# Optimization experiments

Measured on AMD Instinct MI355X. Metric: run time of the kernel, lower is better.

Reference implementation:

```python
import jax, jax.numpy as jnp
import numpy as np

MARGIN = 1.0
EPS = 1e-12


def setup_inputs() -> dict:
    key = jax.random.key(0)
    k1, k2 = jax.random.split(key)
    embeddings = jax.random.normal(k1, (4096, 768), dtype=jnp.float32)
    labels = jax.random.randint(k2, (4096,), 0, 4, dtype=jnp.int64)
    return {"embeddings": embeddings, "labels": labels}


def reference(embeddings, labels):
    # F.normalize(p=2, dim=1): x / max(||x||, eps)
    norm = jnp.linalg.norm(embeddings, axis=1, keepdims=True)
    e = embeddings / jnp.maximum(norm, EPS)

    # Euclidean pairwise distance matrix (not squared)
    dot = e @ e.T                                  # [N, N]
    sq = jnp.diagonal(dot)                         # [N]
    dist = sq[None, :] - 2.0 * dot + sq[:, None]
    dist = jnp.sqrt(jnp.maximum(dist, 0.0) + EPS)  # [N, N]

    # Masks: positives = same label, off-diagonal; negatives = different label
    n = labels.shape[0]
    eq = labels[None, :] == labels[:, None]
    pos_mask = eq & ~jnp.eye(n, dtype=bool)
    neg_mask = ~eq

    # Batch-hard mining: per-anchor hardest positive (masked max) and
    # hardest negative (masked min) -- replaces the per-row Python loop.
    d_ap = jnp.max(jnp.where(pos_mask, dist, -jnp.inf), axis=1)  # [N]
    d_an = jnp.min(jnp.where(neg_mask, dist, jnp.inf), axis=1)   # [N]

    valid = jnp.any(pos_mask, axis=1)  # anchors with at least one positive
    per_anchor = jnp.maximum(d_ap - d_an + MARGIN, 0.0)
    per_anchor = jnp.where(valid, per_anchor, 0.0)
    n_valid = jnp.maximum(jnp.sum(valid.astype(jnp.float32)), 1.0)
    return jnp.sum(per_anchor) / n_valid
```

## Files before the change

kernel.cpp:

```cpp
#include <hip/hip_runtime.h>
#include <math.h>

#define N 4096
#define D 768
#define MARGIN 1.0f
#define NBLK 576
#define NKT 24

typedef _Float16 half8 __attribute__((ext_vector_type(8)));
typedef _Float16 half4 __attribute__((ext_vector_type(4)));
typedef float f32x4 __attribute__((ext_vector_type(4)));

__device__ __forceinline__ void gl2lds16(const void* g, void* l) {
    __builtin_amdgcn_global_load_lds((const __attribute__((address_space(1))) void*)g,
                                     (__attribute__((address_space(3))) void*)l, 16, 0, 0);
}

template<int Nv>
__device__ __forceinline__ void wait_vm() {
    if constexpr (Nv == 0)      asm volatile("s_waitcnt vmcnt(0)" ::: "memory");
    else if constexpr (Nv == 3) asm volatile("s_waitcnt vmcnt(3)" ::: "memory");
    else                        asm volatile("s_waitcnt vmcnt(4)" ::: "memory");
}

__global__ __launch_bounds__(256) void normalize_kernel(const float* __restrict__ x,
                                                        _Float16* __restrict__ e,
                                                        float* __restrict__ sq,
                                                        unsigned* __restrict__ ap_bits,
                                                        unsigned* __restrict__ an_bits,
                                                        unsigned* __restrict__ counter) {
    const int tid = threadIdx.x;
    const int wave = tid >> 6, lane = tid & 63;
    const int row = blockIdx.x * 4 + wave;

    const float4* xr = (const float4*)(x + (size_t)row * D);
    float4 f0 = xr[lane];
    float4 f1 = xr[lane + 64];
    float4 f2 = xr[lane + 128];

    float s = f0.x*f0.x + f0.y*f0.y + f0.z*f0.z + f0.w*f0.w
            + f1.x*f1.x + f1.y*f1.y + f1.z*f1.z + f1.w*f1.w
            + f2.x*f2.x + f2.y*f2.y + f2.z*f2.z + f2.w*f2.w;
    #pragma unroll
    for (int off = 1; off < 64; off <<= 1) s += __shfl_xor(s, off, 64);

    float scale = 1.0f / fmaxf(sqrtf(s), 1e-12f);

    half4* er = (half4*)(e + (size_t)row * D);
    half4 h0 = { (_Float16)(f0.x*scale), (_Float16)(f0.y*scale), (_Float16)(f0.z*scale), (_Float16)(f0.w*scale) };
    half4 h1 = { (_Float16)(f1.x*scale), (_Float16)(f1.y*scale), (_Float16)(f1.z*scale), (_Float16)(f1.w*scale) };
    half4 h2 = { (_Float16)(f2.x*scale), (_Float16)(f2.y*scale), (_Float16)(f2.z*scale), (_Float16)(f2.w*scale) };
    er[lane]       = h0;
    er[lane + 64]  = h1;
    er[lane + 128] = h2;

    if (lane == 0) {
        sq[row] = s * scale * scale;
        ap_bits[row] = 0u;
        an_bits[row] = 0x7f800000u;
    }
    if (blockIdx.x == 0 && tid == 0) *counter = 0u;
}

template<int BROWS>
__device__ __forceinline__ void stage_tile(const _Float16* __restrict__ e,
                                           int i0, int jbase, int k0,
                                           unsigned short* Sb, int tid, int w) {
    #pragma unroll
    for (int p = 0; p < 2; ++p) {
        int s  = p * 256 + tid;
        int r  = s >> 2;
        int kg = (s & 3) ^ ((r >> 1) & 3);
        gl2lds16(e + (size_t)(i0 + r) * D + k0 + kg * 8,
                 (char*)Sb + (p * 256 + w * 64) * 16);
    }
    if constexpr (BROWS == 128) {
        #pragma unroll
        for (int p = 0; p < 2; ++p) {
            int s  = p * 256 + tid;
            int r  = s >> 2;
            int kg = (s & 3) ^ ((r >> 1) & 3);
            gl2lds16(e + (size_t)(jbase + r) * D + k0 + kg * 8,
                     (char*)Sb + 8192 + (p * 256 + w * 64) * 16);
        }
    } else {
        int s  = tid & 127;
        int r  = s >> 2;
        int kg = (s & 3) ^ ((r >> 1) & 3);
        gl2lds16(e + (size_t)(jbase + r) * D + k0 + kg * 8,
                 (char*)Sb + 8192 + ((w & 1) * 64) * 16);
    }
}

template<int MTN, int NTN, int BROWS>
__device__ __forceinline__ void tile_work(const _Float16* __restrict__ e,
                                          const float* __restrict__ sq,
                                          const int* __restrict__ labels,
                                          unsigned* __restrict__ ap_bits,
                                          unsigned* __restrict__ an_bits,
                                          unsigned short* S,
                                          int i0, int jbase,
                                          int wi, int wjL,
                                          int tid, int w, int lane, bool diag) {
    const int ln15 = lane & 15;
    const int lq   = lane >> 4;
    constexpr int LPS = (BROWS == 128) ? 4 : 3;

    f32x4 acc[MTN][NTN] = {};

    stage_tile<BROWS>(e, i0, jbase, 0,  S,        tid, w);
    stage_tile<BROWS>(e, i0, jbase, 32, S + 8192, tid, w);

    int cur = 0, nx2 = 2;
    for (int kt = 0; kt < NKT; ++kt) {
        if (kt < NKT - 1) wait_vm<LPS>(); else wait_vm<0>();
        __builtin_amdgcn_s_barrier();
        __builtin_amdgcn_sched_barrier(0);

        if (kt + 2 < NKT)
            stage_tile<BROWS>(e, i0, jbase, (kt + 2) * 32, S + nx2 * 8192, tid, w);
        __builtin_amdgcn_sched_barrier(0);

        const unsigned short* Sb = S + cur * 8192;
        half8 af[MTN], bf[NTN];
        #pragma unroll
        for (int mt = 0; mt < MTN; ++mt) {
            int r  = wi + mt * 16 + ln15;
            int kx = lq ^ ((r >> 1) & 3);
            af[mt] = *(const half8*)&Sb[r * 32 + kx * 8];
        }
        #pragma unroll
        for (int nt = 0; nt < NTN; ++nt) {
            int r  = wjL + nt * 16 + ln15;
            int kx = lq ^ ((r >> 1) & 3);
            bf[nt] = *(const half8*)&Sb[4096 + r * 32 + kx * 8];
        }
        __builtin_amdgcn_s_setprio(1);
        #pragma unroll
        for (int mt = 0; mt < MTN; ++mt)
            #pragma unroll
            for (int nt = 0; nt < NTN; ++nt)
                acc[mt][nt] = __builtin_amdgcn_mfma_f32_16x16x32_f16(af[mt], bf[nt], acc[mt][nt], 0, 0, 0);
        __builtin_amdgcn_s_setprio(0);

        cur = (cur == 2) ? 0 : cur + 1;
        nx2 = (nx2 == 2) ? 0 : nx2 + 1;
    }

    float sqi[MTN][4]; int labi[MTN][4];
    #pragma unroll
    for (int mt = 0; mt < MTN; ++mt)
        #pragma unroll
        for (int rg = 0; rg < 4; ++rg) {
            int i = i0 + wi + mt * 16 + lq * 4 + rg;
            sqi[mt][rg] = sq[i];
            labi[mt][rg] = labels[i];
        }
    float sqj[NTN]; int labj[NTN];
    #pragma unroll
    for (int nt = 0; nt < NTN; ++nt) {
        int j = jbase + wjL + nt * 16 + ln15;
        sqj[nt] = sq[j];
        labj[nt] = labels[j];
    }

    float api[MTN][4], ani[MTN][4], apj[NTN], anj[NTN];
    #pragma unroll
    for (int mt = 0; mt < MTN; ++mt)
        #pragma unroll
        for (int rg = 0; rg < 4; ++rg) { api[mt][rg] = -INFINITY; ani[mt][rg] = INFINITY; }
    #pragma unroll
    for (int nt = 0; nt < NTN; ++nt) { apj[nt] = -INFINITY; anj[nt] = INFINITY; }

    #pragma unroll
    for (int nt = 0; nt < NTN; ++nt) {
        int j = jbase + wjL + nt * 16 + ln15;
        #pragma unroll
        for (int mt = 0; mt < MTN; ++mt)
            #pragma unroll
            for (int rg = 0; rg < 4; ++rg) {
                int i = i0 + wi + mt * 16 + lq * 4 + rg;
                float d2 = sqi[mt][rg] + sqj[nt] - 2.0f * acc[mt][nt][rg];
                float dist = sqrtf(fmaxf(d2, 0.0f) + 1e-12f);
                if (labi[mt][rg] == labj[nt]) {
                    if (i != j) {
                        api[mt][rg] = fmaxf(api[mt][rg], dist);
                        apj[nt]     = fmaxf(apj[nt], dist);
                    }
                } else {
                    ani[mt][rg] = fminf(ani[mt][rg], dist);
                    anj[nt]     = fminf(anj[nt], dist);
                }
            }
    }

    #pragma unroll
    for (int mt = 0; mt < MTN; ++mt)
        #pragma unroll
        for (int rg = 0; rg < 4; ++rg) {
            float a_ = api[mt][rg], n_ = ani[mt][rg];
            #pragma unroll
            for (int off = 1; off < 16; off <<= 1) {
                a_ = fmaxf(a_, __shfl_xor(a_, off, 64));
                n_ = fminf(n_, __shfl_xor(n_, off, 64));
            }
            if (ln15 == 0) {
                int i = i0 + wi + mt * 16 + lq * 4 + rg;
                if (a_ > -1.0e37f) atomicMax(&ap_bits[i], __float_as_uint(a_));
                if (n_ <  1.0e37f) atomicMin(&an_bits[i], __float_as_uint(n_));
            }
        }

    if (!diag) {
        #pragma unroll
        for (int nt = 0; nt < NTN; ++nt) {
            float a_ = apj[nt], n_ = anj[nt];
            #pragma unroll
            for (int off = 16; off < 64; off <<= 1) {
                a_ = fmaxf(a_, __shfl_xor(a_, off, 64));
                n_ = fminf(n_, __shfl_xor(n_, off, 64));
            }
            if (lq == 0) {
                int j = jbase + wjL + nt * 16 + ln15;
                if (a_ > -1.0e37f) atomicMax(&ap_bits[j], __float_as_uint(a_));
                if (n_ <  1.0e37f) atomicMin(&an_bits[j], __float_as_uint(n_));
            }
        }
    }
}

__global__ __launch_bounds__(256) void mine_kernel(const _Float16* __restrict__ e,
                                                   const float* __restrict__ sq,
                                                   const int* __restrict__ labels,
                                                   unsigned* __restrict__ ap_bits,
                                                   unsigned* __restrict__ an_bits,
                                                   unsigned* __restrict__ counter,
                                                   float* __restrict__ out) {
    __shared__ unsigned short S[3 * 8192];

    const int tid  = threadIdx.x;
    const int w    = tid >> 6;
    const int lane = tid & 63;

    const int b = (blockIdx.x % 8) * 72 + (blockIdx.x / 8);

    int t, jlo, small;
    if (b < 512) { t = b; jlo = 0; small = 0; }
    else { int s2 = b - 512; t = 512 + (s2 >> 2); jlo = (s2 & 3) * 32; small = 1; }

    int bi = 0, rem = t;
    while (rem >= 32 - bi) { rem -= 32 - bi; ++bi; }
    const int bj = bi + rem;
    const int i0 = bi * 128, j0 = bj * 128;

    if (!small)
        tile_work<4, 4, 128>(e, sq, labels, ap_bits, an_bits, S, i0, j0,
                             (w & 1) * 64, (w >> 1) * 64, tid, w, lane, bi == bj);
    else
        tile_work<2, 2, 32>(e, sq, labels, ap_bits, an_bits, S, i0, j0 + jlo,
                            w * 32, 0, tid, w, lane, bi == bj);

    __shared__ unsigned lastFlag;
    __syncthreads();
    if (tid == 0) {
        __builtin_amdgcn_fence(__ATOMIC_RELEASE, "agent");
        lastFlag = (atomicAdd(counter, 1u) == NBLK - 1) ? 1u : 0u;
    }
    __syncthreads();
    if (!lastFlag) return;
    __builtin_amdgcn_fence(__ATOMIC_ACQUIRE, "agent");

    __shared__ int cnt[4];
    __shared__ float red[8];
    if (tid < 4) cnt[tid] = 0;
    __syncthreads();
    int local[4] = {0, 0, 0, 0};
    for (int i = tid; i < N; i += 256) local[labels[i] & 3]++;
    #pragma unroll
    for (int c = 0; c < 4; c++) atomicAdd(&cnt[c], local[c]);
    __syncthreads();

    float sum = 0.f, nv = 0.f;
    for (int i = tid; i < N; i += 256) {
        int l = labels[i] & 3;
        if (cnt[l] >= 2) {
            nv += 1.f;
            float apv = __uint_as_float(ap_bits[i]);
            float anv = __uint_as_float(an_bits[i]);
            if (anv < 3.0e38f) sum += fmaxf(apv - anv + MARGIN, 0.f);
        }
    }

    #pragma unroll
    for (int off = 32; off; off >>= 1) {
        sum += __shfl_down(sum, off, 64);
        nv  += __shfl_down(nv,  off, 64);
    }
    if ((tid & 63) == 0) { red[tid >> 6] = sum; red[4 + (tid >> 6)] = nv; }
    __syncthreads();
    if (tid == 0) {
        float s = red[0] + red[1] + red[2] + red[3];
        float n = red[4] + red[5] + red[6] + red[7];
        out[0] = s / fmaxf(n, 1.f);
    }
}

extern "C" void kernel_launch(void* const* d_in, const int* in_sizes, int n_in,
                              void* d_out, int out_size, void* d_ws, size_t ws_size,
                              hipStream_t stream) {
    const float* x = (const float*)d_in[0];
    const int* labels = (const int*)d_in[1];
    float* out = (float*)d_out;

    _Float16* e = (_Float16*)d_ws;
    float* sq = (float*)(e + (size_t)N * D);
    unsigned* ap_bits = (unsigned*)(sq + N);
    unsigned* an_bits = ap_bits + N;
    unsigned* counter = an_bits + N;

    normalize_kernel<<<N / 4, 256, 0, stream>>>(x, e, sq, ap_bits, an_bits, counter);
    mine_kernel<<<NBLK, 256, 0, stream>>>(e, sq, labels, ap_bits, an_bits, counter, out);
}
```

Baseline: 141.1 us.

## Replace per-row atomics with slot-partitioned partial buffers and separate reduce kernel

Large tiles no longer issue global atomicMax/atomicMin. They first combine row and column extrema across waves in LDS, then write them with plain stores into per-block-row/column slots (32 slots per row). A new reduce kernel folds the slots together with the atomic results from the small tiles, which removes the last-block counter and fence from the mining kernel. The cost is an extra kernel launch, 1 MB of partial buffers that the normalize kernel must initialise, and extra barriers in the tile epilogue.

```diff
diff --git a/kernel.cpp b/kernel.cpp
--- a/kernel.cpp
+++ b/kernel.cpp
@@ -6,6 +6,7 @@
 #define MARGIN 1.0f
 #define NBLK 576
 #define NKT 24
+#define NSLOT 32
 
 typedef _Float16 half8 __attribute__((ext_vector_type(8)));
 typedef _Float16 half4 __attribute__((ext_vector_type(4)));
@@ -28,6 +29,9 @@
                                                         float* __restrict__ sq,
                                                         unsigned* __restrict__ ap_bits,
                                                         unsigned* __restrict__ an_bits,
+                                                        float* __restrict__ ap_part,
+                                                        float* __restrict__ an_part,
+                                                        float* __restrict__ acc,
                                                         unsigned* __restrict__ counter) {
     const int tid = threadIdx.x;
     const int wave = tid >> 6, lane = tid & 63;
@@ -59,7 +63,11 @@
         ap_bits[row] = 0u;
         an_bits[row] = 0x7f800000u;
     }
-    if (blockIdx.x == 0 && tid == 0) *counter = 0u;
+    int g = blockIdx.x * 256 + tid;
+    if (g < NSLOT * N) ap_part[g] = 0.0f;
+    else               an_part[g - NSLOT * N] = INFINITY;
+
+    if (blockIdx.x == 0 && tid == 0) { acc[0] = 0.f; acc[1] = 0.f; *counter = 0u; }
 }
 
 template<int BROWS>
@@ -92,14 +100,17 @@
     }
 }
 
-template<int MTN, int NTN, int BROWS>
+template<int MTN, int NTN, int BROWS, bool SCR>
 __device__ __forceinline__ void tile_work(const _Float16* __restrict__ e,
                                           const float* __restrict__ sq,
                                           const int* __restrict__ labels,
                                           unsigned* __restrict__ ap_bits,
                                           unsigned* __restrict__ an_bits,
+                                          float* __restrict__ ap_part,
+                                          float* __restrict__ an_part,
                                           unsigned short* S,
                                           int i0, int jbase,
+                                          int slot_i, int slot_j,
                                           int wi, int wjL,
                                           int tid, int w, int lane, bool diag) {
     const int ln15 = lane & 15;
@@ -194,36 +205,92 @@
             }
     }
 
-    #pragma unroll
-    for (int mt = 0; mt < MTN; ++mt)
-        #pragma unroll
-        for (int rg = 0; rg < 4; ++rg) {
-            float a_ = api[mt][rg], n_ = ani[mt][rg];
-            #pragma unroll
-            for (int off = 1; off < 16; off <<= 1) {
-                a_ = fmaxf(a_, __shfl_xor(a_, off, 64));
-                n_ = fminf(n_, __shfl_xor(n_, off, 64));
-            }
-            if (ln15 == 0) {
-                int i = i0 + wi + mt * 16 + lq * 4 + rg;
-                if (a_ > -1.0e37f) atomicMax(&ap_bits[i], __float_as_uint(a_));
-                if (n_ <  1.0e37f) atomicMin(&an_bits[i], __float_as_uint(n_));
-            }
-        }
-
-    if (!diag) {
-        #pragma unroll
-        for (int nt = 0; nt < NTN; ++nt) {
-            float a_ = apj[nt], n_ = anj[nt];
-            #pragma unroll
-            for (int off = 16; off < 64; off <<= 1) {
-                a_ = fmaxf(a_, __shfl_xor(a_, off, 64));
-                n_ = fminf(n_, __shfl_xor(n_, off, 64));
-            }
-            if (lq == 0) {
-                int j = jbase + wjL + nt * 16 + ln15;
-                if (a_ > -1.0e37f) atomicMax(&ap_bits[j], __float_as_uint(a_));
-                if (n_ <  1.0e37f) atomicMin(&an_bits[j], __float_as_uint(n_));
+    if constexpr (SCR) {
+        float* F = (float*)S;
+        #pragma unroll
+        for (int mt = 0; mt < MTN; ++mt)
+            #pragma unroll
+            for (int rg = 0; rg < 4; ++rg) {
+                float a_ = api[mt][rg], n_ = ani[mt][rg];
+                #pragma unroll
+                for (int off = 1; off < 16; off <<= 1) {
+                    a_ = fmaxf(a_, __shfl_xor(a_, off, 64));
+                    n_ = fminf(n_, __shfl_xor(n_, off, 64));
+                }
+                if (ln15 == 0) {
+                    int rl = mt * 16 + lq * 4 + rg;
+                    F[w * 128 + rl * 2]     = a_;
+                    F[w * 128 + rl * 2 + 1] = n_;
+                }
+            }
+        __syncthreads();
+        if (tid < 128) {
+            int half = tid >> 6, rl = tid & 63;
+            int wA = half, wB = half + 2;
+            float a_ = fmaxf(F[wA * 128 + rl * 2],     F[wB * 128 + rl * 2]);
+            float n_ = fminf(F[wA * 128 + rl * 2 + 1], F[wB * 128 + rl * 2 + 1]);
+            int row = i0 + half * 64 + rl;
+            ap_part[slot_i * N + row] = a_;
+            an_part[slot_i * N + row] = n_;
+        }
+        if (!diag) {
+            __syncthreads();
+            #pragma unroll
+            for (int nt = 0; nt < NTN; ++nt) {
+                float a_ = apj[nt], n_ = anj[nt];
+                #pragma unroll
+                for (int off = 16; off < 64; off <<= 1) {
+                    a_ = fmaxf(a_, __shfl_xor(a_, off, 64));
+                    n_ = fminf(n_, __shfl_xor(n_, off, 64));
+                }
+                if (lq == 0) {
+                    int jl = nt * 16 + ln15;
+                    F[w * 128 + jl * 2]     = a_;
+                    F[w * 128 + jl * 2 + 1] = n_;
+                }
+            }
+            __syncthreads();
+            if (tid < 128) {
+                int half = tid >> 6, jl = tid & 63;
+                int wA = half * 2, wB = half * 2 + 1;
+                float a_ = fmaxf(F[wA * 128 + jl * 2],     F[wB * 128 + jl * 2]);
+                float n_ = fminf(F[wA * 128 + jl * 2 + 1], F[wB * 128 + jl * 2 + 1]);
+                int col = jbase + half * 64 + jl;
+                ap_part[slot_j * N + col] = a_;
+                an_part[slot_j * N + col] = n_;
+            }
+        }
+    } else {
+        #pragma unroll
+        for (int mt = 0; mt < MTN; ++mt)
+            #pragma unroll
+            for (int rg = 0; rg < 4; ++rg) {
+                float a_ = api[mt][rg], n_ = ani[mt][rg];
+                #pragma unroll
+                for (int off = 1; off < 16; off <<= 1) {
+                    a_ = fmaxf(a_, __shfl_xor(a_, off, 64));
+                    n_ = fminf(n_, __shfl_xor(n_, off, 64));
+                }
+                if (ln15 == 0) {
+                    int i = i0 + wi + mt * 16 + lq * 4 + rg;
+                    if (a_ > -1.0e37f) atomicMax(&ap_bits[i], __float_as_uint(a_));
+                    if (n_ <  1.0e37f) atomicMin(&an_bits[i], __float_as_uint(n_));
+                }
+            }
+        if (!diag) {
+            #pragma unroll
+            for (int nt = 0; nt < NTN; ++nt) {
+                float a_ = apj[nt], n_ = anj[nt];
+                #pragma unroll
+                for (int off = 16; off < 64; off <<= 1) {
+                    a_ = fmaxf(a_, __shfl_xor(a_, off, 64));
+                    n_ = fminf(n_, __shfl_xor(n_, off, 64));
+                }
+                if (lq == 0) {
+                    int j = jbase + wjL + nt * 16 + ln15;
+                    if (a_ > -1.0e37f) atomicMax(&ap_bits[j], __float_as_uint(a_));
+                    if (n_ <  1.0e37f) atomicMin(&an_bits[j], __float_as_uint(n_));
+                }
             }
         }
     }
@@ -234,8 +301,8 @@
                                                    const int* __restrict__ labels,
                                                    unsigned* __restrict__ ap_bits,
                                                    unsigned* __restrict__ an_bits,
-                                                   unsigned* __restrict__ counter,
-                                                   float* __restrict__ out) {
+                                                   float* __restrict__ ap_part,
+                                                   float* __restrict__ an_part) {
     __shared__ unsigned short S[3 * 8192];
 
     const int tid  = threadIdx.x;
@@ -254,21 +321,25 @@
     const int i0 = bi * 128, j0 = bj * 128;
 
     if (!small)
-        tile_work<4, 4, 128>(e, sq, labels, ap_bits, an_bits, S, i0, j0,
-                             (w & 1) * 64, (w >> 1) * 64, tid, w, lane, bi == bj);
+        tile_work<4, 4, 128, true>(e, sq, labels, ap_bits, an_bits, ap_part, an_part, S,
+                                   i0, j0, bj, bi,
+                                   (w & 1) * 64, (w >> 1) * 64, tid, w, lane, bi == bj);
     else
-        tile_work<2, 2, 32>(e, sq, labels, ap_bits, an_bits, S, i0, j0 + jlo,
-                            w * 32, 0, tid, w, lane, bi == bj);
-
-    __shared__ unsigned lastFlag;
-    __syncthreads();
-    if (tid == 0) {
-        __builtin_amdgcn_fence(__ATOMIC_RELEASE, "agent");
-        lastFlag = (atomicAdd(counter, 1u) == NBLK - 1) ? 1u : 0u;
-    }
-    __syncthreads();
-    if (!lastFlag) return;
-    __builtin_amdgcn_fence(__ATOMIC_ACQUIRE, "agent");
+        tile_work<2, 2, 32, false>(e, sq, labels, ap_bits, an_bits, ap_part, an_part, S,
+                                   i0, j0 + jlo, 0, 0,
+                                   w * 32, 0, tid, w, lane, bi == bj);
+}
+
+__global__ __launch_bounds__(256) void reduce_kernel(const float* __restrict__ ap_part,
+                                                     const float* __restrict__ an_part,
+                                                     const unsigned* __restrict__ ap_bits,
+                                                     const unsigned* __restrict__ an_bits,
+                                                     const int* __restrict__ labels,
+                                                     float* __restrict__ acc,
+                                                     unsigned* __restrict__ counter,
+                                                     float* __restrict__ out) {
+    const int tid = threadIdx.x;
+    const int r = blockIdx.x * 256 + tid;
 
     __shared__ int cnt[4];
     __shared__ float red[8];
@@ -277,18 +348,22 @@
     int local[4] = {0, 0, 0, 0};
     for (int i = tid; i < N; i += 256) local[labels[i] & 3]++;
     #pragma unroll
-    for (int c = 0; c < 4; c++) atomicAdd(&cnt[c], local[c]);
+    for (int c = 0; c < 4; c++) if (local[c]) atomicAdd(&cnt[c], local[c]);
     __syncthreads();
 
+    float ap = __uint_as_float(ap_bits[r]);
+    float an = __uint_as_float(an_bits[r]);
+    #pragma unroll
+    for (int s = 0; s < NSLOT; ++s) {
+        ap = fmaxf(ap, ap_part[s * N + r]);
+        an = fminf(an, an_part[s * N + r]);
+    }
+
     float sum = 0.f, nv = 0.f;
-    for (int i = tid; i < N; i += 256) {
-        int l = labels[i] & 3;
-        if (cnt[l] >= 2) {
-            nv += 1.f;
-            float apv = __uint_as_float(ap_bits[i]);
-            float anv = __uint_as_float(an_bits[i]);
-            if (anv < 3.0e38f) sum += fmaxf(apv - anv + MARGIN, 0.f);
-        }
+    int l = labels[r] & 3;
+    if (cnt[l] >= 2) {
+        nv = 1.f;
+        if (an < 3.0e38f) sum = fmaxf(ap - an + MARGIN, 0.f);
     }
 
     #pragma unroll
@@ -299,9 +374,16 @@
     if ((tid & 63) == 0) { red[tid >> 6] = sum; red[4 + (tid >> 6)] = nv; }
     __syncthreads();
     if (tid == 0) {
-        float s = red[0] + red[1] + red[2] + red[3];
-        float n = red[4] + red[5] + red[6] + red[7];
-        out[0] = s / fmaxf(n, 1.f);
+        float bs = red[0] + red[1] + red[2] + red[3];
+        float bn = red[4] + red[5] + red[6] + red[7];
+        atomicAdd(&acc[0], bs);
+        atomicAdd(&acc[1], bn);
+        __threadfence();
+        if (atomicAdd(counter, 1u) == 15u) {
+            float s_ = atomicAdd(&acc[0], 0.f);
+            float n_ = atomicAdd(&acc[1], 0.f);
+            out[0] = s_ / fmaxf(n_, 1.f);
+        }
     }
 }
 
@@ -316,8 +398,14 @@
     float* sq = (float*)(e + (size_t)N * D);
     unsigned* ap_bits = (unsigned*)(sq + N);
     unsigned* an_bits = ap_bits + N;
-    unsigned* counter = an_bits + N;
-
-    normalize_kernel<<<N / 4, 256, 0, stream>>>(x, e, sq, ap_bits, an_bits, counter);
-    mine_kernel<<<NBLK, 256, 0, stream>>>(e, sq, labels, ap_bits, an_bits, counter, out);
-}
+    float* ap_part = (float*)(an_bits + N);
+    float* an_part = ap_part + (size_t)NSLOT * N;
+    float* acc = an_part + (size_t)NSLOT * N;
+    unsigned* counter = (unsigned*)(acc + 2);
+
+    normalize_kernel<<<N / 4, 256, 0, stream>>>(x, e, sq, ap_bits, an_bits,
+                                                ap_part, an_part, acc, counter);
+    mine_kernel<<<NBLK, 256, 0, stream>>>(e, sq, labels, ap_bits, an_bits, ap_part, an_part);
+    reduce_kernel<<<N / 256, 256, 0, stream>>>(ap_part, an_part, ap_bits, an_bits,
+                                               labels, acc, counter, out);
+}
```

Measured after the change: 122.7 us. 1.15x faster.

## Use 128x64 tiles with partial-slot outputs and a separate reduce kernel

Applied to the files above, without the earlier changes.

Replaces the mixed 128x128/128x32 triangular tiling with uniform 128x64 tiles (1056 blocks, launch bounds with 4 blocks per CU, smaller LDS buffers). Per-row and per-column global atomics are replaced by writes into 64 partial slots per row. A new reduce kernel folds the slots and computes the loss, instead of a last-block reduction. The aim is better load balance and occupancy and less atomic contention, at the cost of a third launch, extra partial-buffer traffic, and lower per-block data reuse.

```diff
diff --git a/kernel.cpp b/kernel.cpp
--- a/kernel.cpp
+++ b/kernel.cpp
@@ -4,8 +4,9 @@
 #define N 4096
 #define D 768
 #define MARGIN 1.0f
-#define NBLK 576
+#define NTILE 1056
 #define NKT 24
+#define NSLOT 64
 
 typedef _Float16 half8 __attribute__((ext_vector_type(8)));
 typedef _Float16 half4 __attribute__((ext_vector_type(4)));
@@ -20,14 +21,15 @@
 __device__ __forceinline__ void wait_vm() {
     if constexpr (Nv == 0)      asm volatile("s_waitcnt vmcnt(0)" ::: "memory");
     else if constexpr (Nv == 3) asm volatile("s_waitcnt vmcnt(3)" ::: "memory");
-    else                        asm volatile("s_waitcnt vmcnt(4)" ::: "memory");
+    else                        asm volatile("s_waitcnt vmcnt(6)" ::: "memory");
 }
 
 __global__ __launch_bounds__(256) void normalize_kernel(const float* __restrict__ x,
                                                         _Float16* __restrict__ e,
                                                         float* __restrict__ sq,
-                                                        unsigned* __restrict__ ap_bits,
-                                                        unsigned* __restrict__ an_bits,
+                                                        float* __restrict__ ap_part,
+                                                        float* __restrict__ an_part,
+                                                        float* __restrict__ acc,
                                                         unsigned* __restrict__ counter) {
     const int tid = threadIdx.x;
     const int wave = tid >> 6, lane = tid & 63;
@@ -54,17 +56,17 @@
     er[lane + 64]  = h1;
     er[lane + 128] = h2;
 
-    if (lane == 0) {
-        sq[row] = s * scale * scale;
-        ap_bits[row] = 0u;
-        an_bits[row] = 0x7f800000u;
-    }
-    if (blockIdx.x == 0 && tid == 0) *counter = 0u;
-}
-
-template<int BROWS>
+    if (lane == 0) sq[row] = s * scale * scale;
+
+    int g = blockIdx.x * 256 + tid;
+    ap_part[g] = 0.0f;
+    an_part[g] = INFINITY;
+
+    if (blockIdx.x == 0 && tid == 0) { acc[0] = 0.f; acc[1] = 0.f; *counter = 0u; }
+}
+
 __device__ __forceinline__ void stage_tile(const _Float16* __restrict__ e,
-                                           int i0, int jbase, int k0,
+                                           int i0, int j0, int k0,
                                            unsigned short* Sb, int tid, int w) {
     #pragma unroll
     for (int p = 0; p < 2; ++p) {
@@ -74,72 +76,72 @@
         gl2lds16(e + (size_t)(i0 + r) * D + k0 + kg * 8,
                  (char*)Sb + (p * 256 + w * 64) * 16);
     }
-    if constexpr (BROWS == 128) {
-        #pragma unroll
-        for (int p = 0; p < 2; ++p) {
-            int s  = p * 256 + tid;
-            int r  = s >> 2;
-            int kg = (s & 3) ^ ((r >> 1) & 3);
-            gl2lds16(e + (size_t)(jbase + r) * D + k0 + kg * 8,
-                     (char*)Sb + 8192 + (p * 256 + w * 64) * 16);
-        }
-    } else {
-        int s  = tid & 127;
+    {
+        int s  = tid;
         int r  = s >> 2;
         int kg = (s & 3) ^ ((r >> 1) & 3);
-        gl2lds16(e + (size_t)(jbase + r) * D + k0 + kg * 8,
-                 (char*)Sb + 8192 + ((w & 1) * 64) * 16);
-    }
-}
-
-template<int MTN, int NTN, int BROWS>
-__device__ __forceinline__ void tile_work(const _Float16* __restrict__ e,
-                                          const float* __restrict__ sq,
-                                          const int* __restrict__ labels,
-                                          unsigned* __restrict__ ap_bits,
-                                          unsigned* __restrict__ an_bits,
-                                          unsigned short* S,
-                                          int i0, int jbase,
-                                          int wi, int wjL,
-                                          int tid, int w, int lane, bool diag) {
+        gl2lds16(e + (size_t)(j0 + r) * D + k0 + kg * 8,
+                 (char*)Sb + 8192 + (w * 64) * 16);
+    }
+}
+
+__global__ __launch_bounds__(256, 4) void mine_kernel(const _Float16* __restrict__ e,
+                                                      const float* __restrict__ sq,
+                                                      const int* __restrict__ labels,
+                                                      float* __restrict__ ap_part,
+                                                      float* __restrict__ an_part) {
+    __shared__ unsigned short S[3 * 6144];
+
+    const int tid  = threadIdx.x;
+    const int w    = tid >> 6;
+    const int lane = tid & 63;
     const int ln15 = lane & 15;
     const int lq   = lane >> 4;
-    constexpr int LPS = (BROWS == 128) ? 4 : 3;
-
-    f32x4 acc[MTN][NTN] = {};
-
-    stage_tile<BROWS>(e, i0, jbase, 0,  S,        tid, w);
-    stage_tile<BROWS>(e, i0, jbase, 32, S + 8192, tid, w);
+    const int wr   = w >> 1, wc = w & 1;
+    const int wi   = wr * 64, wjL = wc * 32;
+
+    const int b = (blockIdx.x & 7) * 132 + (blockIdx.x >> 3);
+
+    int bi = 0, rem = b;
+    while (rem >= 64 - 2 * bi) { rem -= 64 - 2 * bi; ++bi; }
+    const int cj = 2 * bi + rem;
+    const bool diag = (rem <= 1);
+    const int i0 = bi * 128, j0 = cj * 64;
+
+    f32x4 acc[4][2] = {};
+
+    stage_tile(e, i0, j0, 0,  S,        tid, w);
+    stage_tile(e, i0, j0, 32, S + 6144, tid, w);
 
     int cur = 0, nx2 = 2;
     for (int kt = 0; kt < NKT; ++kt) {
-        if (kt < NKT - 1) wait_vm<LPS>(); else wait_vm<0>();
+        if (kt < NKT - 1) wait_vm<3>(); else wait_vm<0>();
         __builtin_amdgcn_s_barrier();
         __builtin_amdgcn_sched_barrier(0);
 
         if (kt + 2 < NKT)
-            stage_tile<BROWS>(e, i0, jbase, (kt + 2) * 32, S + nx2 * 8192, tid, w);
+            stage_tile(e, i0, j0, (kt + 2) * 32, S + nx2 * 6144, tid, w);
         __builtin_amdgcn_sched_barrier(0);
 
-        const unsigned short* Sb = S + cur * 8192;
-        half8 af[MTN], bf[NTN];
-        #pragma unroll
-        for (int mt = 0; mt < MTN; ++mt) {
+        const unsigned short* Sb = S + cur * 6144;
+        half8 af[4], bf[2];
+        #pragma unroll
+        for (int mt = 0; mt < 4; ++mt) {
             int r  = wi + mt * 16 + ln15;
             int kx = lq ^ ((r >> 1) & 3);
             af[mt] = *(const half8*)&Sb[r * 32 + kx * 8];
         }
         #pragma unroll
-        for (int nt = 0; nt < NTN; ++nt) {
-            int r  = wjL + nt * 16 + ln15;
-            int kx = lq ^ ((r >> 1) & 3);
-            bf[nt] = *(const half8*)&Sb[4096 + r * 32 + kx * 8];
+        for (int nt = 0; nt < 2; ++nt) {
+            int c  = wjL + nt * 16 + ln15;
+            int kx = lq ^ ((c >> 1) & 3);
+            bf[nt] = *(const half8*)&Sb[4096 + c * 32 + kx * 8];
         }
         __builtin_amdgcn_s_setprio(1);
         #pragma unroll
-        for (int mt = 0; mt < MTN; ++mt)
+        for (int mt = 0; mt < 4; ++mt)
             #pragma unroll
-            for (int nt = 0; nt < NTN; ++nt)
+            for (int nt = 0; nt < 2; ++nt)
                 acc[mt][nt] = __builtin_amdgcn_mfma_f32_16x16x32_f16(af[mt], bf[nt], acc[mt][nt], 0, 0, 0);
         __builtin_amdgcn_s_setprio(0);
 
@@ -147,36 +149,36 @@
         nx2 = (nx2 == 2) ? 0 : nx2 + 1;
     }
 
-    float sqi[MTN][4]; int labi[MTN][4];
-    #pragma unroll
-    for (int mt = 0; mt < MTN; ++mt)
+    float sqi[4][4]; int labi[4][4];
+    #pragma unroll
+    for (int mt = 0; mt < 4; ++mt)
         #pragma unroll
         for (int rg = 0; rg < 4; ++rg) {
             int i = i0 + wi + mt * 16 + lq * 4 + rg;
             sqi[mt][rg] = sq[i];
             labi[mt][rg] = labels[i];
         }
-    float sqj[NTN]; int labj[NTN];
-    #pragma unroll
-    for (int nt = 0; nt < NTN; ++nt) {
-        int j = jbase + wjL + nt * 16 + ln15;
+    float sqj[2]; int labj[2];
+    #pragma unroll
+    for (int nt = 0; nt < 2; ++nt) {
+        int j = j0 + wjL + nt * 16 + ln15;
         sqj[nt] = sq[j];
         labj[nt] = labels[j];
     }
 
-    float api[MTN][4], ani[MTN][4], apj[NTN], anj[NTN];
-    #pragma unroll
-    for (int mt = 0; mt < MTN; ++mt)
+    float api[4][4], ani[4][4], apj[2], anj[2];
+    #pragma unroll
+    for (int mt = 0; mt < 4; ++mt)
         #pragma unroll
         for (int rg = 0; rg < 4; ++rg) { api[mt][rg] = -INFINITY; ani[mt][rg] = INFINITY; }
     #pragma unroll
-    for (int nt = 0; nt < NTN; ++nt) { apj[nt] = -INFINITY; anj[nt] = INFINITY; }
-
-    #pragma unroll
-    for (int nt = 0; nt < NTN; ++nt) {
-        int j = jbase + wjL + nt * 16 + ln15;
-        #pragma unroll
-        for (int mt = 0; mt < MTN; ++mt)
+    for (int nt = 0; nt < 2; ++nt) { apj[nt] = -INFINITY; anj[nt] = INFINITY; }
+
+    #pragma unroll
+    for (int nt = 0; nt < 2; ++nt) {
+        int j = j0 + wjL + nt * 16 + ln15;
+        #pragma unroll
+        for (int mt = 0; mt < 4; ++mt)
             #pragma unroll
             for (int rg = 0; rg < 4; ++rg) {
                 int i = i0 + wi + mt * 16 + lq * 4 + rg;
@@ -194,8 +196,10 @@
             }
     }
 
-    #pragma unroll
-    for (int mt = 0; mt < MTN; ++mt)
+    float* F = (float*)S;
+
+    #pragma unroll
+    for (int mt = 0; mt < 4; ++mt)
         #pragma unroll
         for (int rg = 0; rg < 4; ++rg) {
             float a_ = api[mt][rg], n_ = ani[mt][rg];
@@ -205,15 +209,25 @@
                 n_ = fminf(n_, __shfl_xor(n_, off, 64));
             }
             if (ln15 == 0) {
-                int i = i0 + wi + mt * 16 + lq * 4 + rg;
-                if (a_ > -1.0e37f) atomicMax(&ap_bits[i], __float_as_uint(a_));
-                if (n_ <  1.0e37f) atomicMin(&an_bits[i], __float_as_uint(n_));
-            }
-        }
+                int rl = mt * 16 + lq * 4 + rg;
+                F[w * 128 + rl * 2]     = a_;
+                F[w * 128 + rl * 2 + 1] = n_;
+            }
+        }
+    __syncthreads();
+    if (tid < 128) {
+        int half = tid >> 6, rl = tid & 63;
+        float a_ = fmaxf(F[(2 * half) * 128 + rl * 2],     F[(2 * half + 1) * 128 + rl * 2]);
+        float n_ = fminf(F[(2 * half) * 128 + rl * 2 + 1], F[(2 * half + 1) * 128 + rl * 2 + 1]);
+        int row = i0 + half * 64 + rl;
+        ap_part[(size_t)cj * N + row] = a_;
+        an_part[(size_t)cj * N + row] = n_;
+    }
 
     if (!diag) {
-        #pragma unroll
-        for (int nt = 0; nt < NTN; ++nt) {
+        __syncthreads();
+        #pragma unroll
+        for (int nt = 0; nt < 2; ++nt) {
             float a_ = apj[nt], n_ = anj[nt];
             #pragma unroll
             for (int off = 16; off < 64; off <<= 1) {
@@ -221,87 +235,78 @@
                 n_ = fminf(n_, __shfl_xor(n_, off, 64));
             }
             if (lq == 0) {
-                int j = jbase + wjL + nt * 16 + ln15;
-                if (a_ > -1.0e37f) atomicMax(&ap_bits[j], __float_as_uint(a_));
-                if (n_ <  1.0e37f) atomicMin(&an_bits[j], __float_as_uint(n_));
-            }
-        }
-    }
-}
-
-__global__ __launch_bounds__(256) void mine_kernel(const _Float16* __restrict__ e,
-                                                   const float* __restrict__ sq,
-                                                   const int* __restrict__ labels,
-                                                   unsigned* __restrict__ ap_bits,
-                                                   unsigned* __restrict__ an_bits,
-                                                   unsigned* __restrict__ counter,
-                                                   float* __restrict__ out) {
-    __shared__ unsigned short S[3 * 8192];
-
-    const int tid  = threadIdx.x;
-    const int w    = tid >> 6;
-    const int lane = tid & 63;
-
-    const int b = (blockIdx.x % 8) * 72 + (blockIdx.x / 8);
-
-    int t, jlo, small;
-    if (b < 512) { t = b; jlo = 0; small = 0; }
-    else { int s2 = b - 512; t = 512 + (s2 >> 2); jlo = (s2 & 3) * 32; small = 1; }
-
-    int bi = 0, rem = t;
-    while (rem >= 32 - bi) { rem -= 32 - bi; ++bi; }
-    const int bj = bi + rem;
-    const int i0 = bi * 128, j0 = bj * 128;
-
-    if (!small)
-        tile_work<4, 4, 128>(e, sq, labels, ap_bits, an_bits, S, i0, j0,
-                             (w & 1) * 64, (w >> 1) * 64, tid, w, lane, bi == bj);
-    else
-        tile_work<2, 2, 32>(e, sq, labels, ap_bits, an_bits, S, i0, j0 + jlo,
-                            w * 32, 0, tid, w, lane, bi == bj);
-
-    __shared__ unsigned lastFlag;
-    __syncthreads();
-    if (tid == 0) {
-        __builtin_amdgcn_fence(__ATOMIC_RELEASE, "agent");
-        lastFlag = (atomicAdd(counter, 1u) == NBLK - 1) ? 1u : 0u;
-    }
-    __syncthreads();
-    if (!lastFlag) return;
-    __builtin_amdgcn_fence(__ATOMIC_ACQUIRE, "agent");
+                int jl = nt * 16 + ln15;
+                F[w * 128 + jl * 2]     = a_;
+                F[w * 128 + jl * 2 + 1] = n_;
+            }
+        }
+        __syncthreads();
+        if (tid < 64) {
+            int wc2 = tid >> 5, jl = tid & 31;
+            float a_ = fmaxf(F[wc2 * 128 + jl * 2],     F[(wc2 + 2) * 128 + jl * 2]);
+            float n_ = fminf(F[wc2 * 128 + jl * 2 + 1], F[(wc2 + 2) * 128 + jl * 2 + 1]);
+            int col = j0 + wc2 * 32 + jl;
+            ap_part[(size_t)bi * N + col] = a_;
+            an_part[(size_t)bi * N + col] = n_;
+        }
+    }
+}
+
+__global__ __launch_bounds__(256) void reduce_kernel(const float* __restrict__ ap_part,
+                                                     const float* __restrict__ an_part,
+                                                     const int* __restrict__ labels,
+                                                     float* __restrict__ acc,
+                                                     unsigned* __restrict__ counter,
+                                                     float* __restrict__ out) {
+    const int tid = threadIdx.x;
+    const int rl  = tid & 63;
+    const int q   = tid >> 6;
+    const int r   = blockIdx.x * 64 + rl;
 
     __shared__ int cnt[4];
-    __shared__ float red[8];
+    __shared__ float Fa[4][64], Fn[4][64];
     if (tid < 4) cnt[tid] = 0;
     __syncthreads();
     int local[4] = {0, 0, 0, 0};
     for (int i = tid; i < N; i += 256) local[labels[i] & 3]++;
     #pragma unroll
-    for (int c = 0; c < 4; c++) atomicAdd(&cnt[c], local[c]);
+    for (int c = 0; c < 4; c++) if (local[c]) atomicAdd(&cnt[c], local[c]);
+
+    float ap = 0.0f, an = INFINITY;
+    #pragma unroll
+    for (int s = 0; s < 16; ++s) {
+        int slot = q * 16 + s;
+        ap = fmaxf(ap, ap_part[(size_t)slot * N + r]);
+        an = fminf(an, an_part[(size_t)slot * N + r]);
+    }
+    Fa[q][rl] = ap; Fn[q][rl] = an;
     __syncthreads();
 
-    float sum = 0.f, nv = 0.f;
-    for (int i = tid; i < N; i += 256) {
-        int l = labels[i] & 3;
+    if (tid < 64) {
+        float a_ = fmaxf(fmaxf(Fa[0][tid], Fa[1][tid]), fmaxf(Fa[2][tid], Fa[3][tid]));
+        float n_ = fminf(fminf(Fn[0][tid], Fn[1][tid]), fminf(Fn[2][tid], Fn[3][tid]));
+        int row = blockIdx.x * 64 + tid;
+        int l = labels[row] & 3;
+        float sum = 0.f, nv = 0.f;
         if (cnt[l] >= 2) {
-            nv += 1.f;
-            float apv = __uint_as_float(ap_bits[i]);
-            float anv = __uint_as_float(an_bits[i]);
-            if (anv < 3.0e38f) sum += fmaxf(apv - anv + MARGIN, 0.f);
-        }
-    }
-
-    #pragma unroll
-    for (int off = 32; off; off >>= 1) {
-        sum += __shfl_down(sum, off, 64);
-        nv  += __shfl_down(nv,  off, 64);
-    }
-    if ((tid & 63) == 0) { red[tid >> 6] = sum; red[4 + (tid >> 6)] = nv; }
-    __syncthreads();
-    if (tid == 0) {
-        float s = red[0] + red[1] + red[2] + red[3];
-        float n = red[4] + red[5] + red[6] + red[7];
-        out[0] = s / fmaxf(n, 1.f);
+            nv = 1.f;
+            if (n_ < 3.0e38f) sum = fmaxf(a_ - n_ + MARGIN, 0.f);
+        }
+        #pragma unroll
+        for (int off = 32; off; off >>= 1) {
+            sum += __shfl_down(sum, off, 64);
+            nv  += __shfl_down(nv,  off, 64);
+        }
+        if (tid == 0) {
+            atomicAdd(&acc[0], sum);
+            atomicAdd(&acc[1], nv);
+            __threadfence();
+            if (atomicAdd(counter, 1u) == 63u) {
+                float s_ = atomicAdd(&acc[0], 0.f);
+                float nn = atomicAdd(&acc[1], 0.f);
+                out[0] = s_ / fmaxf(nn, 1.f);
+            }
+        }
     }
 }
 
@@ -314,10 +319,12 @@
 
     _Float16* e = (_Float16*)d_ws;
     float* sq = (float*)(e + (size_t)N * D);
-    unsigned* ap_bits = (unsigned*)(sq + N);
-    unsigned* an_bits = ap_bits + N;
-    unsigned* counter = an_bits + N;
-
-    normalize_kernel<<<N / 4, 256, 0, stream>>>(x, e, sq, ap_bits, an_bits, counter);
-    mine_kernel<<<NBLK, 256, 0, stream>>>(e, sq, labels, ap_bits, an_bits, counter, out);
-}
+    float* ap_part = sq + N;
+    float* an_part = ap_part + (size_t)NSLOT * N;
+    float* acc = an_part + (size_t)NSLOT * N;
+    unsigned* counter = (unsigned*)(acc + 2);
+
+    normalize_kernel<<<N / 4, 256, 0, stream>>>(x, e, sq, ap_part, an_part, acc, counter);
+    mine_kernel<<<NTILE, 256, 0, stream>>>(e, sq, labels, ap_part, an_part);
+    reduce_kernel<<<N / 64, 256, 0, stream>>>(ap_part, an_part, labels, acc, counter, out);
+}
```

After: 116.5 us. -17.4%, faster.
